# Performance work log

Hardware: AMD Instinct MI355X
Metric: run time of the kernel (lower is better)

The kernel has to match this reference:

```python
import jax, jax.numpy as jnp
import numpy as np

B, NS, NN = 1024, 1, 64
F = 128            # feat_dim = edge_dim = time_dim = pos_dim
DM = 4 * F         # model_dim = 512
H, DK = 2, 256     # n_head, d_k = d_v = model_dim // n_head
LN_EPS = 1e-5


def setup_inputs() -> dict:
    key = jax.random.key(0)
    ks = jax.random.split(key, 20)
    s = 0.02
    inp = {
        'src':   jax.random.normal(ks[0], (B, NS, F), jnp.float32),
        'src_t': jax.random.normal(ks[1], (B, NS, F), jnp.float32),
        'src_p': jax.random.normal(ks[2], (B, NS, F), jnp.float32),
        'seq':   jax.random.normal(ks[3], (B, NN, F), jnp.float32),
        'seq_t': jax.random.normal(ks[4], (B, NN, F), jnp.float32),
        'seq_e': jax.random.normal(ks[5], (B, NN, F), jnp.float32),
        'seq_p': jax.random.normal(ks[6], (B, NN, F), jnp.float32),
        'mask':  jax.random.randint(ks[7], (B, NS, NN), 0, 2).astype(bool),
        # MapBasedMultiHeadAttention params
        'wq': jax.random.normal(ks[8], (H * DK, DM), jnp.float32) * s,
        'wk': jax.random.normal(ks[9], (H * DK, DM), jnp.float32) * s,
        'wv': jax.random.normal(ks[10], (H * DK, DM), jnp.float32) * s,
        'wm': jax.random.normal(ks[11], (2 * DK,), jnp.float32) * s,   # weight_map: Linear(2*d_k, 1, bias=False)
        'fc_w': jax.random.normal(ks[12], (DM, H * DK), jnp.float32) * s,
        'fc_b': jnp.zeros((DM,), jnp.float32),
        'ln_g': jnp.ones((DM,), jnp.float32),
        'ln_b': jnp.zeros((DM,), jnp.float32),
        # MergeLayer(model_dim, feat_dim, feat_dim, feat_dim)
        'm1_w': jax.random.normal(ks[13], (F, DM + F), jnp.float32) * s,
        'm1_b': jnp.zeros((F,), jnp.float32),
        'm2_w': jax.random.normal(ks[14], (F, F), jnp.float32) * s,
        'm2_b': jnp.zeros((F,), jnp.float32),
    }
    return inp


def reference(src, src_t, src_p, seq, seq_t, seq_e, seq_p, mask,
              wq, wk, wv, wm, fc_w, fc_b, ln_g, ln_b, m1_w, m1_b, m2_w, m2_b):
    b, ns, f = src.shape
    nn = seq.shape[1]
    src_e = jnp.zeros((b, ns, f), src.dtype)  # edge feats of sources are zero
    q = jnp.concatenate([src, src_e, src_t, src_p], axis=-1)   # [B,NS,DM]
    k = jnp.concatenate([seq, seq_e, seq_t, seq_p], axis=-1)   # [B,NN,DM]

    # per-head projections: weight [H*DK, DM] -> [H, DK, DM]
    qh = jnp.einsum('bsd,hed->bshe', q, wq.reshape(H, DK, DM))  # [B,NS,H,DK]
    kh = jnp.einsum('bnd,hed->bnhe', k, wk.reshape(H, DK, DM))  # [B,NN,H,DK]
    vh = jnp.einsum('bnd,hed->bnhe', k, wv.reshape(H, DK, DM))  # [B,NN,H,DK]

    # weight_map(Linear over concat([q,k])) == q @ wm[:DK] + k @ wm[DK:]
    score_q = jnp.einsum('bshe,e->bhs', qh, wm[:DK])            # [B,H,NS]
    score_k = jnp.einsum('bnhe,e->bhn', kh, wm[DK:])            # [B,H,NN]
    attn = score_q[..., None] + score_k[:, :, None, :]          # [B,H,NS,NN]
    attn = jnp.where(mask[:, None, :, :], jnp.float32(-1e10), attn)
    attn = jax.nn.softmax(attn, axis=-1)

    out = jnp.einsum('bhsn,bnhe->bshe', attn, vh).reshape(b, ns, H * DK)
    out = jnp.einsum('bsd,ed->bse', out, fc_w) + fc_b           # fc
    out = jnp.where(out >= 0, out, 0.2 * out)                   # LeakyReLU(0.2)
    out = out + q                                               # residual
    mu = out.mean(axis=-1, keepdims=True)
    var = out.var(axis=-1, keepdims=True)
    out = (out - mu) / jnp.sqrt(var + LN_EPS) * ln_g + ln_b     # LayerNorm

    # MergeLayer (non_linear=True)
    x = jnp.concatenate([out, src], axis=-1)                    # [B,NS,DM+F]
    hdn = jax.nn.relu(jnp.einsum('bsd,ed->bse', x, m1_w) + m1_b)
    z = jnp.einsum('bsd,ed->bse', hdn, m2_w) + m2_b             # [B,NS,F]

    # attn in original layout: [n_head*B, len_q, len_k]
    attn_flat = attn.transpose(1, 0, 2, 3).reshape(H * b, ns, nn)
    return (z, attn_flat)
```

## Files before the change

kernel.cpp:

```cpp
#include <hip/hip_runtime.h>
#include <hip/hip_bf16.h>
#include <stdint.h>

#define B_   1024
#define NN_  64
#define F_   128
#define DM_  512
#define DK_  256

typedef unsigned short u16;
using f32x4  = __attribute__((ext_vector_type(4))) float;
using bf16x8 = __attribute__((ext_vector_type(8))) short;

__device__ __forceinline__ uint32_t f2bf(float x) {
  uint32_t u = __builtin_bit_cast(uint32_t, x);
  return (u + 0x7fffu + ((u >> 16) & 1u)) >> 16;
}
__device__ __forceinline__ float bf2f(uint32_t us) {
  return __builtin_bit_cast(float, us << 16);
}
__device__ __forceinline__ void split_pack(float x, float y, uint32_t& hp, uint32_t& lp) {
  uint32_t hx = f2bf(x), hy = f2bf(y);
  uint32_t lx = f2bf(x - bf2f(hx)), ly = f2bf(y - bf2f(hy));
  hp = hx | (hy << 16);
  lp = lx | (ly << 16);
}
__device__ __forceinline__ void split1(float x, u16& h, u16& l) {
  uint32_t hx = f2bf(x);
  h = (u16)hx;
  l = (u16)f2bf(x - bf2f(hx));
}
__device__ __forceinline__ float dpp_xor1(float x) {
  int r = __builtin_amdgcn_mov_dpp(__builtin_bit_cast(int, x), 0xB1, 0xF, 0xF, true);
  return __builtin_bit_cast(float, r);
}
__device__ __forceinline__ float dpp_xor2(float x) {
  int r = __builtin_amdgcn_mov_dpp(__builtin_bit_cast(int, x), 0x4E, 0xF, 0xF, true);
  return __builtin_bit_cast(float, r);
}

__global__ __launch_bounds__(256) void k_wkc(
    const float* __restrict__ wk, const float* __restrict__ wm,
    float* __restrict__ wkc) {
  __shared__ float part[4][64];
  int h = blockIdx.x >> 3, dc = blockIdx.x & 7;
  int w = threadIdx.x >> 6, l = threadIdx.x & 63;
  int d = dc * 64 + l;
  const float* base = wk + (size_t)(h * DK_ + w * 64) * DM_ + d;
  float sacc[8] = {0.f, 0.f, 0.f, 0.f, 0.f, 0.f, 0.f, 0.f};
  #pragma unroll
  for (int e = 0; e < 64; ++e)
    sacc[e & 7] += base[e * DM_] * wm[DK_ + w * 64 + e];
  float s = ((sacc[0] + sacc[1]) + (sacc[2] + sacc[3])) +
            ((sacc[4] + sacc[5]) + (sacc[6] + sacc[7]));
  part[w][l] = s;
  __syncthreads();
  if (w == 0)
    wkc[h * DM_ + d] = part[0][l] + part[1][l] + part[2][l] + part[3][l];
}

__global__ __launch_bounds__(256) void k_prep(
    const float* __restrict__ wv, const float* __restrict__ fc_w,
    const float* __restrict__ m1_w, const float* __restrict__ m2_w,
    u16* __restrict__ fc_hi, u16* __restrict__ fc_lo,
    u16* __restrict__ wvT_hi, u16* __restrict__ wvT_lo,
    u16* __restrict__ m1_hi, u16* __restrict__ m1_lo,
    u16* __restrict__ m2_hi, u16* __restrict__ m2_lo) {
  __shared__ float tile[32][33];
  int tid = threadIdx.x;
  int bx = blockIdx.x;
  int gtid = bx * 256 + tid;
  int nthr = gridDim.x * 256;

  for (int i = gtid; i < DM_ * DM_; i += nthr) split1(fc_w[i], fc_hi[i], fc_lo[i]);
  for (int i = gtid; i < F_ * (DM_ + F_); i += nthr) split1(m1_w[i], m1_hi[i], m1_lo[i]);
  for (int i = gtid; i < F_ * F_; i += nthr) split1(m2_w[i], m2_hi[i], m2_lo[i]);

  int e0 = (bx >> 4) * 32, d0 = (bx & 15) * 32;
  int rr = tid >> 3, c4 = (tid & 7) * 4;
  float4 v = *(const float4*)(wv + (e0 + rr) * DM_ + d0 + c4);
  tile[rr][c4] = v.x; tile[rr][c4 + 1] = v.y;
  tile[rr][c4 + 2] = v.z; tile[rr][c4 + 3] = v.w;
  __syncthreads();
  int dr = tid >> 3, ec = (tid & 7) * 4;
  #pragma unroll
  for (int q = 0; q < 4; ++q) {
    int idx = (d0 + dr) * DM_ + e0 + ec + q;
    split1(tile[ec + q][dr], wvT_hi[idx], wvT_lo[idx]);
  }
}

__device__ __forceinline__ f32x4 mfma_tile_split(
    const u16* __restrict__ Ahi, const u16* __restrict__ Alo, int lda,
    const u16* __restrict__ Bhi, const u16* __restrict__ Blo, int ldb, int K) {
  int l = threadIdx.x & 63;
  int r = l & 15, g = l >> 4;
  int offA = r * lda + g * 8;
  int offB = r * ldb + g * 8;
  f32x4 acc = {0.f, 0.f, 0.f, 0.f};
  for (int k = 0; k < K; k += 32) {
    bf16x8 ah = *(const bf16x8*)(Ahi + offA + k);
    bf16x8 al = *(const bf16x8*)(Alo + offA + k);
    bf16x8 bh = *(const bf16x8*)(Bhi + offB + k);
    bf16x8 bl = *(const bf16x8*)(Blo + offB + k);
    acc = __builtin_amdgcn_mfma_f32_16x16x32_bf16(ah, bh, acc, 0, 0, 0);
    acc = __builtin_amdgcn_mfma_f32_16x16x32_bf16(ah, bl, acc, 0, 0, 0);
    acc = __builtin_amdgcn_mfma_f32_16x16x32_bf16(al, bh, acc, 0, 0, 0);
  }
  return acc;
}

__global__ __launch_bounds__(256) void k_wcomb(
    const u16* __restrict__ fc_hi, const u16* __restrict__ fc_lo,
    const u16* __restrict__ wvT_hi, const u16* __restrict__ wvT_lo,
    u16* __restrict__ wc_hi, u16* __restrict__ wc_lo) {
  int wid = threadIdx.x >> 6;
  int n0g = blockIdx.y * 32;
  int h = n0g >> 9, d0 = n0g & 511;
  int m0 = blockIdx.x * 32 + (wid >> 1) * 16;
  int nb = d0 + (wid & 1) * 16;
  f32x4 acc = mfma_tile_split(fc_hi + m0 * DM_ + h * DK_,
                              fc_lo + m0 * DM_ + h * DK_, DM_,
                              wvT_hi + nb * DM_ + h * DK_,
                              wvT_lo + nb * DM_ + h * DK_, DM_, DK_);
  int l = threadIdx.x & 63, r = l & 15, g = l >> 4;
  #pragma unroll
  for (int i = 0; i < 4; ++i) {
    int m = m0 + g * 4 + i;
    int idx = m * 1024 + n0g + (wid & 1) * 16 + r;
    split1(acc[i], wc_hi[idx], wc_lo[idx]);
  }
}

__global__ __launch_bounds__(256) void k_attn(
    const float* __restrict__ seq, const float* __restrict__ seq_e,
    const float* __restrict__ seq_t, const float* __restrict__ seq_p,
    const int* __restrict__ mask, const float* __restrict__ wkc,
    float* __restrict__ attn_out,
    uint32_t* __restrict__ kbar_hi, uint32_t* __restrict__ kbar_lo) {
  __shared__ float pbuf[4][2][64][17];
  __shared__ float attns[2][64];
  int tid = threadIdx.x, b = blockIdx.x;
  int w = tid >> 6, i = tid & 63;

  const float* arr = (w == 0 ? seq : (w == 1 ? seq_e : (w == 2 ? seq_t : seq_p)));
  const float* base = arr + (size_t)b * (64 * 128) + 2 * i;
  float c00 = wkc[w * 128 + 2 * i],       c01 = wkc[w * 128 + 2 * i + 1];
  float c10 = wkc[512 + w * 128 + 2 * i], c11 = wkc[512 + w * 128 + 2 * i + 1];

  float kx[64], ky[64];
  #pragma unroll
  for (int j = 0; j < 64; ++j) {
    float2 v = *(const float2*)(base + j * 128);
    kx[j] = v.x; ky[j] = v.y;
  }
  #pragma unroll
  for (int j = 0; j < 64; ++j) {
    float p0 = kx[j] * c00 + ky[j] * c01;
    float p1 = kx[j] * c10 + ky[j] * c11;
    p0 += dpp_xor1(p0); p0 += dpp_xor2(p0);
    p1 += dpp_xor1(p1); p1 += dpp_xor2(p1);
    if ((i & 3) == 0) {
      pbuf[w][0][j][i >> 2] = p0;
      pbuf[w][1][j][i >> 2] = p1;
    }
  }
  __syncthreads();

  if (tid < 128) {
    int h = w;
    float s = 0.f;
    #pragma unroll
    for (int w4 = 0; w4 < 4; ++w4)
      #pragma unroll
      for (int gq = 0; gq < 16; ++gq) s += pbuf[w4][h][i][gq];
    if (mask[b * 64 + i]) s = -1e10f;
    float m = s;
    #pragma unroll
    for (int off = 32; off; off >>= 1) m = fmaxf(m, __shfl_xor(m, off));
    float p = expf(s - m);
    float ssum = p;
    #pragma unroll
    for (int off = 32; off; off >>= 1) ssum += __shfl_xor(ssum, off);
    float a = p / ssum;
    attns[h][i] = a;
    attn_out[(h * B_ + b) * 64 + i] = a;
  }
  __syncthreads();

  float a00 = 0.f, a01 = 0.f, a10 = 0.f, a11 = 0.f;
  #pragma unroll
  for (int j = 0; j < 64; ++j) {
    float t0 = attns[0][j], t1 = attns[1][j];
    a00 += t0 * kx[j]; a01 += t0 * ky[j];
    a10 += t1 * kx[j]; a11 += t1 * ky[j];
  }
  uint32_t hp, lp;
  int idx = b * 512 + w * 64 + i;
  split_pack(a00, a01, hp, lp);
  kbar_hi[idx] = hp; kbar_lo[idx] = lp;
  split_pack(a10, a11, hp, lp);
  kbar_hi[idx + 256] = hp; kbar_lo[idx + 256] = lp;
}

__global__ __launch_bounds__(256) void k_fc(
    const u16* __restrict__ kb_hi, const u16* __restrict__ kb_lo,
    const u16* __restrict__ wc_hi, const u16* __restrict__ wc_lo,
    const float* __restrict__ fc_b,
    const float* __restrict__ src, const float* __restrict__ src_t,
    const float* __restrict__ src_p, float* __restrict__ fco) {
  int tid = threadIdx.x;
  int wid = tid >> 6, l = tid & 63;
  int r = l & 15, g = l >> 4;
  int m0 = blockIdx.x * 32 + (wid >> 1) * 16;
  int n0 = blockIdx.y * 64 + (wid & 1) * 32;
  int offA  = (m0 + r) * 1024 + g * 8;
  int offB0 = (n0 + r) * 1024 + g * 8;
  int offB1 = offB0 + 16 * 1024;
  f32x4 acc0 = {0.f, 0.f, 0.f, 0.f}, acc1 = {0.f, 0.f, 0.f, 0.f};
  #pragma unroll 4
  for (int k = 0; k < 1024; k += 32) {
    bf16x8 ah  = *(const bf16x8*)(kb_hi + offA + k);
    bf16x8 al  = *(const bf16x8*)(kb_lo + offA + k);
    bf16x8 b0h = *(const bf16x8*)(wc_hi + offB0 + k);
    bf16x8 b0l = *(const bf16x8*)(wc_lo + offB0 + k);
    bf16x8 b1h = *(const bf16x8*)(wc_hi + offB1 + k);
    bf16x8 b1l = *(const bf16x8*)(wc_lo + offB1 + k);
    acc0 = __builtin_amdgcn_mfma_f32_16x16x32_bf16(ah, b0h, acc0, 0, 0, 0);
    acc0 = __builtin_amdgcn_mfma_f32_16x16x32_bf16(ah, b0l, acc0, 0, 0, 0);
    acc0 = __builtin_amdgcn_mfma_f32_16x16x32_bf16(al, b0h, acc0, 0, 0, 0);
    acc1 = __builtin_amdgcn_mfma_f32_16x16x32_bf16(ah, b1h, acc1, 0, 0, 0);
    acc1 = __builtin_amdgcn_mfma_f32_16x16x32_bf16(ah, b1l, acc1, 0, 0, 0);
    acc1 = __builtin_amdgcn_mfma_f32_16x16x32_bf16(al, b1h, acc1, 0, 0, 0);
  }
  #pragma unroll
  for (int f = 0; f < 2; ++f) {
    int col = n0 + f * 16 + r;
    int part = col >> 7, fc2 = col & 127;
    float bias = fc_b[col];
    const float* qsrc = (part == 0 ? src : (part == 2 ? src_t : src_p));
    #pragma unroll
    for (int i = 0; i < 4; ++i) {
      int m = m0 + g * 4 + i;
      float c = (f == 0 ? acc0[i] : acc1[i]) + bias;
      c = (c >= 0.f) ? c : 0.2f * c;
      float qv = (part == 1) ? 0.f : qsrc[m * 128 + fc2];
      fco[m * 512 + col] = c + qv;
    }
  }
}

__global__ __launch_bounds__(64) void k_ln(
    const float* __restrict__ fco, const float* __restrict__ ln_g,
    const float* __restrict__ ln_b, const float* __restrict__ src,
    u16* __restrict__ x_hi, u16* __restrict__ x_lo) {
  int b = blockIdx.x, l = threadIdx.x;
  float v[8];
  float s = 0.f, s2 = 0.f;
  #pragma unroll
  for (int j = 0; j < 8; ++j) {
    v[j] = fco[b * 512 + j * 64 + l];
    s += v[j]; s2 += v[j] * v[j];
  }
  #pragma unroll
  for (int off = 32; off; off >>= 1) { s += __shfl_xor(s, off); s2 += __shfl_xor(s2, off); }
  float mu = s * (1.f / 512.f);
  float var = s2 * (1.f / 512.f) - mu * mu;
  float rstd = rsqrtf(var + 1e-5f);
  #pragma unroll
  for (int j = 0; j < 8; ++j) {
    int idx = j * 64 + l;
    float o = (v[j] - mu) * rstd * ln_g[idx] + ln_b[idx];
    int xi = b * 640 + idx;
    split1(o, x_hi[xi], x_lo[xi]);
  }
  #pragma unroll
  for (int j = 0; j < 2; ++j) {
    int xi = b * 640 + 512 + j * 64 + l;
    split1(src[b * 128 + j * 64 + l], x_hi[xi], x_lo[xi]);
  }
}

__global__ __launch_bounds__(512) void k_m12(
    const u16* __restrict__ x_hi, const u16* __restrict__ x_lo,
    const u16* __restrict__ m1_hi, const u16* __restrict__ m1_lo,
    const float* __restrict__ m1_b,
    const u16* __restrict__ m2_hi, const u16* __restrict__ m2_lo,
    const float* __restrict__ m2_b, float* __restrict__ z) {
  __shared__ u16 hh[16][136], hl[16][136];
  int tid = threadIdx.x;
  int wid = tid >> 6, l = tid & 63;
  int r = l & 15, g = l >> 4;
  int m0 = blockIdx.x * 16;
  int nb = wid * 16;
  {
    f32x4 acc = mfma_tile_split(x_hi + m0 * 640, x_lo + m0 * 640, 640,
                                m1_hi + nb * 640, m1_lo + nb * 640, 640, 640);
    int col = nb + r;
    float bias = m1_b[col];
    #pragma unroll
    for (int ii = 0; ii < 4; ++ii) {
      int row = g * 4 + ii;
      float o = fmaxf(acc[ii] + bias, 0.f);
      split1(o, hh[row][col], hl[row][col]);
    }
  }
  __syncthreads();
  {
    f32x4 acc = mfma_tile_split(&hh[0][0], &hl[0][0], 136,
                                m2_hi + nb * 128, m2_lo + nb * 128, 128, 128);
    int col = nb + r;
    float bias = m2_b[col];
    #pragma unroll
    for (int ii = 0; ii < 4; ++ii) {
      int row = g * 4 + ii;
      z[(m0 + row) * 128 + col] = acc[ii] + bias;
    }
  }
}

extern "C" void kernel_launch(void* const* d_in, const int* in_sizes, int n_in,
                              void* d_out, int out_size, void* d_ws, size_t ws_size,
                              hipStream_t stream) {
  (void)in_sizes; (void)n_in; (void)out_size; (void)ws_size;
  const float* src   = (const float*)d_in[0];
  const float* src_t = (const float*)d_in[1];
  const float* src_p = (const float*)d_in[2];
  const float* seq   = (const float*)d_in[3];
  const float* seq_t = (const float*)d_in[4];
  const float* seq_e = (const float*)d_in[5];
  const float* seq_p = (const float*)d_in[6];
  const int*   mask  = (const int*)d_in[7];
  const float* wk   = (const float*)d_in[9];
  const float* wv   = (const float*)d_in[10];
  const float* wm   = (const float*)d_in[11];
  const float* fc_w = (const float*)d_in[12];
  const float* fc_b = (const float*)d_in[13];
  const float* ln_g = (const float*)d_in[14];
  const float* ln_b = (const float*)d_in[15];
  const float* m1_w = (const float*)d_in[16];
  const float* m1_b = (const float*)d_in[17];
  const float* m2_w = (const float*)d_in[18];
  const float* m2_b = (const float*)d_in[19];

  float* z_out    = (float*)d_out;
  float* attn_out = z_out + B_ * F_;

  char* ws = (char*)d_ws;
  float* wkc     = (float*)(ws + 0);
  u16* fc_hi     = (u16*)(ws + 4096);
  u16* fc_lo     = (u16*)(ws + 528384);
  u16* m1_hi     = (u16*)(ws + 1052672);
  u16* m1_lo     = (u16*)(ws + 1216512);
  u16* m2_hi     = (u16*)(ws + 1380352);
  u16* m2_lo     = (u16*)(ws + 1413120);
  u16* wvT_hi    = (u16*)(ws + 1445888);
  u16* wvT_lo    = (u16*)(ws + 1970176);
  u16* wc_hi     = (u16*)(ws + 2494464);
  u16* wc_lo     = (u16*)(ws + 3543040);
  uint32_t* kbhi = (uint32_t*)(ws + 4591616);
  uint32_t* kblo = (uint32_t*)(ws + 6688768);
  float* fco     = (float*)(ws + 8785920);
  u16* x_hi      = (u16*)(ws + 10883072);
  u16* x_lo      = (u16*)(ws + 12193792);

  hipLaunchKernelGGL(k_wkc, dim3(16), dim3(256), 0, stream, wk, wm, wkc);
  hipLaunchKernelGGL(k_prep, dim3(256), dim3(256), 0, stream,
                     wv, fc_w, m1_w, m2_w,
                     fc_hi, fc_lo, wvT_hi, wvT_lo,
                     m1_hi, m1_lo, m2_hi, m2_lo);
  hipLaunchKernelGGL(k_attn, dim3(1024), dim3(256), 0, stream,
                     seq, seq_e, seq_t, seq_p, mask, wkc,
                     attn_out, kbhi, kblo);
  hipLaunchKernelGGL(k_wcomb, dim3(16, 32), dim3(256), 0, stream,
                     fc_hi, fc_lo, wvT_hi, wvT_lo, wc_hi, wc_lo);
  hipLaunchKernelGGL(k_fc, dim3(32, 8), dim3(256), 0, stream,
                     (const u16*)kbhi, (const u16*)kblo, wc_hi, wc_lo, fc_b,
                     src, src_t, src_p, fco);
  hipLaunchKernelGGL(k_ln, dim3(1024), dim3(64), 0, stream,
                     fco, ln_g, ln_b, src, x_hi, x_lo);
  hipLaunchKernelGGL(k_m12, dim3(64), dim3(512), 0, stream,
                     x_hi, x_lo, m1_hi, m1_lo, m1_b, m2_hi, m2_lo, m2_b, z_out);
}
```

Baseline: 95.88 us.

## Widen DPP reduction to 16 lanes and drop register-cached K rows in attention

The attention-score kernel now reduces each partial dot product across 16 lanes with DPP row_shr steps instead of 4, so only one lane in 16 writes to shared memory. The shared partial buffer shrinks and the final per-key sum reads 16 values instead of 64. The 128-register kx/ky cache is removed, and the weighted-sum pass reloads the K rows from global memory (likely L2/L1 hits). This cuts register pressure and LDS traffic at the cost of a second read of the input rows.

```diff
diff --git a/kernel.cpp b/kernel.cpp
--- a/kernel.cpp
+++ b/kernel.cpp
@@ -30,13 +30,17 @@
   h = (u16)hx;
   l = (u16)f2bf(x - bf2f(hx));
 }
-__device__ __forceinline__ float dpp_xor1(float x) {
-  int r = __builtin_amdgcn_mov_dpp(__builtin_bit_cast(int, x), 0xB1, 0xF, 0xF, true);
-  return __builtin_bit_cast(float, r);
-}
-__device__ __forceinline__ float dpp_xor2(float x) {
-  int r = __builtin_amdgcn_mov_dpp(__builtin_bit_cast(int, x), 0x4E, 0xF, 0xF, true);
-  return __builtin_bit_cast(float, r);
+template <int CTRL>
+__device__ __forceinline__ float dppadd(float x) {
+  int r = __builtin_amdgcn_mov_dpp(__builtin_bit_cast(int, x), CTRL, 0xF, 0xF, true);
+  return x + __builtin_bit_cast(float, r);
+}
+__device__ __forceinline__ float red16(float p) {
+  p = dppadd<0xB1>(p);
+  p = dppadd<0x4E>(p);
+  p = dppadd<0x114>(p);
+  p = dppadd<0x118>(p);
+  return p;
 }
 
 __global__ __launch_bounds__(256) void k_wkc(
@@ -138,7 +142,7 @@
     const int* __restrict__ mask, const float* __restrict__ wkc,
     float* __restrict__ attn_out,
     uint32_t* __restrict__ kbar_hi, uint32_t* __restrict__ kbar_lo) {
-  __shared__ float pbuf[4][2][64][17];
+  __shared__ float pbuf[4][2][64][5];
   __shared__ float attns[2][64];
   int tid = threadIdx.x, b = blockIdx.x;
   int w = tid >> 6, i = tid & 63;
@@ -148,21 +152,14 @@
   float c00 = wkc[w * 128 + 2 * i],       c01 = wkc[w * 128 + 2 * i + 1];
   float c10 = wkc[512 + w * 128 + 2 * i], c11 = wkc[512 + w * 128 + 2 * i + 1];
 
-  float kx[64], ky[64];
   #pragma unroll
   for (int j = 0; j < 64; ++j) {
     float2 v = *(const float2*)(base + j * 128);
-    kx[j] = v.x; ky[j] = v.y;
-  }
-  #pragma unroll
-  for (int j = 0; j < 64; ++j) {
-    float p0 = kx[j] * c00 + ky[j] * c01;
-    float p1 = kx[j] * c10 + ky[j] * c11;
-    p0 += dpp_xor1(p0); p0 += dpp_xor2(p0);
-    p1 += dpp_xor1(p1); p1 += dpp_xor2(p1);
-    if ((i & 3) == 0) {
-      pbuf[w][0][j][i >> 2] = p0;
-      pbuf[w][1][j][i >> 2] = p1;
+    float p0 = red16(v.x * c00 + v.y * c01);
+    float p1 = red16(v.x * c10 + v.y * c11);
+    if ((i & 15) == 12) {
+      pbuf[w][0][j][i >> 4] = p0;
+      pbuf[w][1][j][i >> 4] = p1;
     }
   }
   __syncthreads();
@@ -173,7 +170,7 @@
     #pragma unroll
     for (int w4 = 0; w4 < 4; ++w4)
       #pragma unroll
-      for (int gq = 0; gq < 16; ++gq) s += pbuf[w4][h][i][gq];
+      for (int gq = 0; gq < 4; ++gq) s += pbuf[w4][h][i][gq];
     if (mask[b * 64 + i]) s = -1e10f;
     float m = s;
     #pragma unroll
@@ -191,9 +188,10 @@
   float a00 = 0.f, a01 = 0.f, a10 = 0.f, a11 = 0.f;
   #pragma unroll
   for (int j = 0; j < 64; ++j) {
+    float2 v = *(const float2*)(base + j * 128);
     float t0 = attns[0][j], t1 = attns[1][j];
-    a00 += t0 * kx[j]; a01 += t0 * ky[j];
-    a10 += t1 * kx[j]; a11 += t1 * ky[j];
+    a00 += t0 * v.x; a01 += t0 * v.y;
+    a10 += t1 * v.x; a11 += t1 * v.y;
   }
   uint32_t hp, lp;
   int idx = b * 512 + w * 64 + i;
```

Result: slower. 135.5 us (+41.4%).
